# Optimization experiments

Measured on AMD Instinct MI355X. Metric: run time of the kernel, lower is better.

## Reference

```python
import jax, jax.numpy as jnp
import numpy as np

# Dimensions: B volumes, S=15 slices, C=16 channels, H=W=6 spatial (hardcoded in module)
B, S, C, H, W = 4096, 15, 16, 6, 6
N_LUNG, N_HEART = 28, 27
N_OUT = 2 * N_LUNG + N_HEART  # 83
IN_FEAT = C * H * W           # 576


def setup_inputs() -> dict:
    key = jax.random.key(0)
    k0, k1, k2, k3, k4 = jax.random.split(key, 5)
    x = jax.random.normal(k0, (B, S, C, H, W), dtype=jnp.float32)
    dzfeatweights_heart = jax.random.normal(k1, (1, N_HEART, C, 1, 1), dtype=jnp.float32)
    dzfeatweights_lung = jax.random.normal(k2, (1, N_LUNG, C, 1, 1), dtype=jnp.float32)
    bound = 1.0 / np.sqrt(IN_FEAT)  # kaiming/fan_in style init bound
    fclayers_weights = jax.random.uniform(k3, (N_OUT, IN_FEAT), minval=-bound, maxval=bound, dtype=jnp.float32)
    fclayers_biases = jax.random.uniform(k4, (N_OUT,), minval=-bound, maxval=bound, dtype=jnp.float32)
    return {"x": x,
            "dzfeatweights_heart": dzfeatweights_heart,
            "dzfeatweights_lung": dzfeatweights_lung,
            "fclayers_weights": fclayers_weights,
            "fclayers_biases": fclayers_biases}


def reference(x, dzfeatweights_heart, dzfeatweights_lung, fclayers_weights, fclayers_biases):
    # x: [B, S, C, H, W] post-backbone features (one row per CT volume)
    Bc, Sc, Cc, Hc, Wc = x.shape
    # nonlinearity='softmax' -> Softmax(dim=2), i.e. over the 16 channels
    attn_heart = jax.nn.softmax(dzfeatweights_heart[0, :, :, 0, 0], axis=1)  # [n_heart, C]
    attn_lung = jax.nn.softmax(dzfeatweights_lung[0, :, :, 0, 0], axis=1)    # [n_lung, C]
    # disease order in the original cat: heart, left lung, right lung (lung weights shared)
    attn = jnp.concatenate([attn_heart, attn_lung, attn_lung], axis=0)       # [O, C]
    # Fuse the channel-attention broadcast-mul into the per-disease FC weights:
    # pred[b,s,o] = sum_{c,h,w} x[b,s,c,h,w] * attn[o,c] * Wfc[o,c,h,w] + bias[o]
    Wfc = fclayers_weights.reshape(-1, Cc, Hc, Wc)                           # [O, C, H, W]
    Weff = attn[:, :, None, None] * Wfc                                      # [O, C, H, W]
    slice_preds = jnp.einsum('bschw,ochw->bso', x, Weff) + fclayers_biases   # [B, S, O]
    # AvgPool1d(kernel_size=slices) over the slice axis -> [B, O]
    return jnp.mean(slice_preds, axis=1)
```

## Files before the change

### kernel.cpp

```cpp
#include <hip/hip_runtime.h>

#define NOUT 83
#define NHEART 27
#define NLUNG 28

__global__ __launch_bounds__(384, 2) void bodyavg_fused8(
    const float4* __restrict__ x4,
    const float* __restrict__ dzh,
    const float* __restrict__ dzl,
    const float4* __restrict__ fcw4,
    const float* __restrict__ fcb,
    float* __restrict__ out,
    int B)
{
    __shared__ float  attn_lds[NOUT * 17];
    __shared__ float4 xms[8 * 144];

    const int tid = threadIdx.x;
    const int blk = blockIdx.x;
    const int b0  = blk * 8;

    if (tid < NOUT) {
        const int o = tid;
        const float* row = (o < NHEART) ? (dzh + o * 16)
                                        : (dzl + ((o - NHEART) % NLUNG) * 16);
        float vals[16];
        #pragma unroll
        for (int c = 0; c < 16; ++c) vals[c] = row[c];
        float m = vals[0];
        #pragma unroll
        for (int c = 1; c < 16; ++c) m = fmaxf(m, vals[c]);
        float s = 0.f;
        #pragma unroll
        for (int c = 0; c < 16; ++c) { vals[c] = expf(vals[c] - m); s += vals[c]; }
        const float inv = 1.0f / s;
        #pragma unroll
        for (int c = 0; c < 16; ++c) attn_lds[o * 17 + c] = vals[c] * inv;
    }

    const float4* xb = x4 + (size_t)b0 * 2160;
    #pragma unroll
    for (int r = 0; r < 3; ++r) {
        const int p = tid + r * 384;
        const int v = p / 144;
        const int q = p - v * 144;
        if (b0 + v < B) {
            const float4* src = xb + v * 2160 + q;
            float4 t[15];
            #pragma unroll
            for (int s = 0; s < 15; ++s) t[s] = src[s * 144];
            float sx = 0.f, sy = 0.f, sz = 0.f, sw = 0.f;
            #pragma unroll
            for (int s = 0; s < 15; ++s) {
                sx += t[s].x; sy += t[s].y; sz += t[s].z; sw += t[s].w;
            }
            const float sc = 1.0f / 15.0f;
            xms[p] = make_float4(sx * sc, sy * sc, sz * sc, sw * sc);
        } else {
            xms[p] = make_float4(0.f, 0.f, 0.f, 0.f);
        }
    }
    __syncthreads();

    const int grp = tid >> 4;
    const int l   = tid & 15;

    int oc[4];
    const float4* wr[4];
    #pragma unroll
    for (int k = 0; k < 4; ++k) {
        const int o = grp + 24 * k;
        oc[k] = (o < NOUT) ? o : 0;
        wr[k] = fcw4 + oc[k] * 144;
    }

    float acc[4][8] = {};

    #pragma unroll 3
    for (int jj = 0; jj < 9; ++jj) {
        const int q  = l + 16 * jj;
        const int cc = q / 9;

        float4 xv[8];
        #pragma unroll
        for (int v = 0; v < 8; ++v) xv[v] = xms[v * 144 + q];

        #pragma unroll
        for (int k = 0; k < 4; ++k) {
            const float4 w = wr[k][q];
            const float  a = attn_lds[oc[k] * 17 + cc];
            const float wx = a * w.x, wy = a * w.y, wz = a * w.z, ww = a * w.w;
            #pragma unroll
            for (int v = 0; v < 8; ++v) {
                acc[k][v] = fmaf(wx, xv[v].x, acc[k][v]);
                acc[k][v] = fmaf(wy, xv[v].y, acc[k][v]);
                acc[k][v] = fmaf(wz, xv[v].z, acc[k][v]);
                acc[k][v] = fmaf(ww, xv[v].w, acc[k][v]);
            }
        }
    }

    #pragma unroll
    for (int k = 0; k < 4; ++k) {
        float r4[4];
        #pragma unroll
        for (int j = 0; j < 4; ++j) {
            const float lo = acc[k][2 * j], hi = acc[k][2 * j + 1];
            const bool  up = (l & 1);
            const float keep = up ? hi : lo;
            const float send = up ? lo : hi;
            r4[j] = keep + __shfl_xor(send, 1, 16);
        }
        float r2[2];
        #pragma unroll
        for (int j = 0; j < 2; ++j) {
            const float lo = r4[2 * j], hi = r4[2 * j + 1];
            const bool  up = (l & 2);
            const float keep = up ? hi : lo;
            const float send = up ? lo : hi;
            r2[j] = keep + __shfl_xor(send, 2, 16);
        }
        float r1;
        {
            const float lo = r2[0], hi = r2[1];
            const bool  up = (l & 4);
            const float keep = up ? hi : lo;
            const float send = up ? lo : hi;
            r1 = keep + __shfl_xor(send, 4, 16);
        }
        r1 += __shfl_xor(r1, 8, 16);

        const int o = grp + 24 * k;
        const int b = b0 + (l & 7);
        if (l < 8 && o < NOUT && b < B)
            out[(size_t)b * NOUT + o] = r1 + fcb[o];
    }
}

extern "C" void kernel_launch(void* const* d_in, const int* in_sizes, int n_in,
                              void* d_out, int out_size, void* d_ws, size_t ws_size,
                              hipStream_t stream) {
    const float* x   = (const float*)d_in[0];
    const float* dzh = (const float*)d_in[1];
    const float* dzl = (const float*)d_in[2];
    const float* fcw = (const float*)d_in[3];
    const float* fcb = (const float*)d_in[4];
    float* out = (float*)d_out;

    const int B = in_sizes[0] / (15 * 16 * 6 * 6);
    const int blocks = (B + 7) / 8;

    hipLaunchKernelGGL(bodyavg_fused8, dim3(blocks), dim3(384), 0, stream,
                       reinterpret_cast<const float4*>(x), dzh, dzl,
                       reinterpret_cast<const float4*>(fcw), fcb, out, B);
}
```

Measured before the change: 38.76 us.

## Stream each volume contiguously per wavefront and fold slice-mean scale into attention

Each 64-lane wavefront now owns one batch volume and reads its 2160 float4 values as one contiguous coalesced stream. It accumulates into 9 periodic register slots and then folds them into the shared slice-mean buffer. Previously each thread gathered 15 slice values at a stride of 144 float4. The 1/15 averaging factor moves into the softmax attention weights. The block grows to 512 threads with 3 output groups per thread instead of 4. The read-modify-write into LDS relies on in-order execution within the wave for overlapping slots.

```diff
diff --git a/kernel.cpp b/kernel.cpp
--- a/kernel.cpp
+++ b/kernel.cpp
@@ -4,7 +4,7 @@
 #define NHEART 27
 #define NLUNG 28
 
-__global__ __launch_bounds__(384, 2) void bodyavg_fused8(
+__global__ __launch_bounds__(512) void bodyavg_scan8(
     const float4* __restrict__ x4,
     const float* __restrict__ dzh,
     const float* __restrict__ dzl,
@@ -33,52 +33,85 @@
         float s = 0.f;
         #pragma unroll
         for (int c = 0; c < 16; ++c) { vals[c] = expf(vals[c] - m); s += vals[c]; }
-        const float inv = 1.0f / s;
+        const float inv = (1.0f / s) * (1.0f / 15.0f);
         #pragma unroll
         for (int c = 0; c < 16; ++c) attn_lds[o * 17 + c] = vals[c] * inv;
     }
 
-    const float4* xb = x4 + (size_t)b0 * 2160;
+    const int w = tid >> 6;
+    const int l = tid & 63;
+    const int b = b0 + w;
+
+    {
+        const float4 z = make_float4(0.f, 0.f, 0.f, 0.f);
+        xms[w * 144 + l] = z;
+        xms[w * 144 + l + 64] = z;
+        if (l < 16) xms[w * 144 + l + 128] = z;
+    }
+
+    float4 acc[9];
     #pragma unroll
-    for (int r = 0; r < 3; ++r) {
-        const int p = tid + r * 384;
-        const int v = p / 144;
-        const int q = p - v * 144;
-        if (b0 + v < B) {
-            const float4* src = xb + v * 2160 + q;
-            float4 t[15];
+    for (int j = 0; j < 9; ++j) acc[j] = make_float4(0.f, 0.f, 0.f, 0.f);
+
+    if (b < B) {
+        const float4* src = x4 + (size_t)b * 2160 + l;
+        #pragma unroll
+        for (int c = 0; c < 3; ++c) {
+            float4 t[9];
             #pragma unroll
-            for (int s = 0; s < 15; ++s) t[s] = src[s * 144];
-            float sx = 0.f, sy = 0.f, sz = 0.f, sw = 0.f;
+            for (int u = 0; u < 9; ++u) t[u] = src[(c * 9 + u) * 64];
             #pragma unroll
-            for (int s = 0; s < 15; ++s) {
-                sx += t[s].x; sy += t[s].y; sz += t[s].z; sw += t[s].w;
+            for (int u = 0; u < 9; ++u) {
+                acc[u].x += t[u].x; acc[u].y += t[u].y;
+                acc[u].z += t[u].z; acc[u].w += t[u].w;
             }
-            const float sc = 1.0f / 15.0f;
-            xms[p] = make_float4(sx * sc, sy * sc, sz * sc, sw * sc);
-        } else {
-            xms[p] = make_float4(0.f, 0.f, 0.f, 0.f);
+        }
+        {
+            float4 t[6];
+            #pragma unroll
+            for (int u = 0; u < 6; ++u) t[u] = src[(27 + u) * 64];
+            #pragma unroll
+            for (int u = 0; u < 6; ++u) {
+                acc[u].x += t[u].x; acc[u].y += t[u].y;
+                acc[u].z += t[u].z; acc[u].w += t[u].w;
+            }
+        }
+        if (l < 48) {
+            const float4 t = src[33 * 64];
+            acc[6].x += t.x; acc[6].y += t.y; acc[6].z += t.z; acc[6].w += t.w;
         }
     }
+
+    #pragma unroll
+    for (int j = 0; j < 9; ++j) {
+        int p = (64 * j) % 144 + l;
+        if (p >= 144) p -= 144;
+        const int idx = w * 144 + p;
+        float4 cur = xms[idx];
+        cur.x += acc[j].x; cur.y += acc[j].y;
+        cur.z += acc[j].z; cur.w += acc[j].w;
+        xms[idx] = cur;
+    }
+
     __syncthreads();
 
     const int grp = tid >> 4;
-    const int l   = tid & 15;
+    const int ll  = tid & 15;
 
-    int oc[4];
-    const float4* wr[4];
+    int oc[3];
+    const float4* wr[3];
     #pragma unroll
-    for (int k = 0; k < 4; ++k) {
-        const int o = grp + 24 * k;
+    for (int k = 0; k < 3; ++k) {
+        const int o = grp + 32 * k;
         oc[k] = (o < NOUT) ? o : 0;
         wr[k] = fcw4 + oc[k] * 144;
     }
 
-    float acc[4][8] = {};
+    float facc[3][8] = {};
 
     #pragma unroll 3
     for (int jj = 0; jj < 9; ++jj) {
-        const int q  = l + 16 * jj;
+        const int q  = ll + 16 * jj;
         const int cc = q / 9;
 
         float4 xv[8];
@@ -86,27 +119,27 @@
         for (int v = 0; v < 8; ++v) xv[v] = xms[v * 144 + q];
 
         #pragma unroll
-        for (int k = 0; k < 4; ++k) {
-            const float4 w = wr[k][q];
-            const float  a = attn_lds[oc[k] * 17 + cc];
-            const float wx = a * w.x, wy = a * w.y, wz = a * w.z, ww = a * w.w;
+        for (int k = 0; k < 3; ++k) {
+            const float4 wq = wr[k][q];
+            const float  a  = attn_lds[oc[k] * 17 + cc];
+            const float wx = a * wq.x, wy = a * wq.y, wz = a * wq.z, ww = a * wq.w;
             #pragma unroll
             for (int v = 0; v < 8; ++v) {
-                acc[k][v] = fmaf(wx, xv[v].x, acc[k][v]);
-                acc[k][v] = fmaf(wy, xv[v].y, acc[k][v]);
-                acc[k][v] = fmaf(wz, xv[v].z, acc[k][v]);
-                acc[k][v] = fmaf(ww, xv[v].w, acc[k][v]);
+                facc[k][v] = fmaf(wx, xv[v].x, facc[k][v]);
+                facc[k][v] = fmaf(wy, xv[v].y, facc[k][v]);
+                facc[k][v] = fmaf(wz, xv[v].z, facc[k][v]);
+                facc[k][v] = fmaf(ww, xv[v].w, facc[k][v]);
             }
         }
     }
 
     #pragma unroll
-    for (int k = 0; k < 4; ++k) {
+    for (int k = 0; k < 3; ++k) {
         float r4[4];
         #pragma unroll
         for (int j = 0; j < 4; ++j) {
-            const float lo = acc[k][2 * j], hi = acc[k][2 * j + 1];
-            const bool  up = (l & 1);
+            const float lo = facc[k][2 * j], hi = facc[k][2 * j + 1];
+            const bool  up = (ll & 1);
             const float keep = up ? hi : lo;
             const float send = up ? lo : hi;
             r4[j] = keep + __shfl_xor(send, 1, 16);
@@ -115,7 +148,7 @@
         #pragma unroll
         for (int j = 0; j < 2; ++j) {
             const float lo = r4[2 * j], hi = r4[2 * j + 1];
-            const bool  up = (l & 2);
+            const bool  up = (ll & 2);
             const float keep = up ? hi : lo;
             const float send = up ? lo : hi;
             r2[j] = keep + __shfl_xor(send, 2, 16);
@@ -123,17 +156,17 @@
         float r1;
         {
             const float lo = r2[0], hi = r2[1];
-            const bool  up = (l & 4);
+            const bool  up = (ll & 4);
             const float keep = up ? hi : lo;
             const float send = up ? lo : hi;
             r1 = keep + __shfl_xor(send, 4, 16);
         }
         r1 += __shfl_xor(r1, 8, 16);
 
-        const int o = grp + 24 * k;
-        const int b = b0 + (l & 7);
-        if (l < 8 && o < NOUT && b < B)
-            out[(size_t)b * NOUT + o] = r1 + fcb[o];
+        const int o = grp + 32 * k;
+        const int bb = b0 + (ll & 7);
+        if (ll < 8 && o < NOUT && bb < B)
+            out[(size_t)bb * NOUT + o] = r1 + fcb[o];
     }
 }
 
@@ -150,7 +183,7 @@
     const int B = in_sizes[0] / (15 * 16 * 6 * 6);
     const int blocks = (B + 7) / 8;
 
-    hipLaunchKernelGGL(bodyavg_fused8, dim3(blocks), dim3(384), 0, stream,
+    hipLaunchKernelGGL(bodyavg_scan8, dim3(blocks), dim3(512), 0, stream,
                        reinterpret_cast<const float4*>(x), dzh, dzl,
                        reinterpret_cast<const float4*>(fcw), fcb, out, B);
 }
```

Result: faster. 34.98 us (-9.7%).
